# Kernel tuning notes

Hardware: AMD Instinct MI355X
Metric: run time of the kernel (lower is better)

Reference implementation:

```python
import jax, jax.numpy as jnp
import numpy as np

G = 8      # conv groups
NG = 32    # groupnorm groups
H = 8      # attention heads
EPS = 1e-5
SLOPE = 0.1

def _qkv_branch(x, w, b, gw, gb):
    # x: [B, Cin, P]; w: [Cout, Cin//G]; grouped 1x1 conv == block matmul
    B, Cin, P = x.shape
    Cout = w.shape[0]
    xg = x.reshape(B, G, Cin // G, P)
    wg = w.reshape(G, Cout // G, Cin // G)
    y = jnp.einsum('gof,bgfp->bgop', wg, xg).reshape(B, Cout, P) + b[None, :, None]
    # GroupNorm(NG, Cout)
    yg = y.reshape(B, NG, Cout // NG, P)
    mu = yg.mean(axis=(2, 3), keepdims=True)
    var = yg.var(axis=(2, 3), keepdims=True)
    yn = ((yg - mu) * jax.lax.rsqrt(var + EPS)).reshape(B, Cout, P)
    yn = yn * gw[None, :, None] + gb[None, :, None]
    # LeakyReLU(0.1)
    return jnp.where(yn >= 0, yn, SLOPE * yn)

def setup_inputs() -> dict:
    key = jax.random.key(0)
    ks = jax.random.split(key, 14)
    B, Cin, Cout, P = 8, 512, 1024, 2048
    x = jax.random.normal(ks[0], (B, Cin, P), dtype=jnp.float32)
    def conv_w(k):
        return jax.random.normal(k, (Cout, Cin // G), dtype=jnp.float32) * 0.02
    inp = {
        'x': x,
        'wq': conv_w(ks[1]), 'bq': jnp.zeros((Cout,), jnp.float32),
        'gw1': jnp.ones((Cout,), jnp.float32), 'gb1': jnp.zeros((Cout,), jnp.float32),
        'wk': conv_w(ks[2]), 'bk': jnp.zeros((Cout,), jnp.float32),
        'gw2': jnp.ones((Cout,), jnp.float32), 'gb2': jnp.zeros((Cout,), jnp.float32),
        'wv': conv_w(ks[3]), 'bv': jnp.zeros((Cout,), jnp.float32),
        'gw3': jnp.ones((Cout,), jnp.float32), 'gb3': jnp.zeros((Cout,), jnp.float32),
    }
    return inp

def reference(x, wq, bq, gw1, gb1, wk, bk, gw2, gb2, wv, bv, gw3, gb3):
    Q = _qkv_branch(x, wq, bq, gw1, gb1)   # [B, C, P]
    K = _qkv_branch(x, wk, bk, gw2, gb2)
    V = _qkv_branch(x, wv, bv, gw3, gb3)
    B, C, P = K.shape
    d = C // H
    Qh = Q.reshape(B, H, d, P)
    Kh = K.reshape(B, H, d, P)
    Vh = V.reshape(B, H, d, P)
    scale = 1.0 / np.sqrt(C / H).astype(np.float32)
    scores = jnp.einsum('bhci,bhcj->bhij', Kh, Vh) * scale  # [B,H,P,P]
    A = jax.nn.softmax(scores, axis=-1)
    out = jnp.einsum('bhij,bhcj->bhci', A, Qh)              # [B,H,d,P]
    return out.reshape(B, C, P)
```

## Files before the change

### kernel.cpp

```cpp
#include <hip/hip_runtime.h>

typedef unsigned short ushort_t;
typedef float  f32x4   __attribute__((ext_vector_type(4)));
typedef float  f32x16  __attribute__((ext_vector_type(16)));
typedef __bf16 bf16x4  __attribute__((ext_vector_type(4)));
typedef __bf16 bf16x8  __attribute__((ext_vector_type(8)));

#define MFMA16(a,b,c) __builtin_amdgcn_mfma_f32_16x16x32_bf16((a),(b),(c),0,0,0)
#define MFMA32(a,b,c) __builtin_amdgcn_mfma_f32_32x32x16_bf16((a),(b),(c),0,0,0)

__device__ __forceinline__ ushort_t f2bf(float f) {
  union { float f; unsigned u; } v; v.f = f;
  unsigned u = v.u;
  unsigned r = u + 0x7FFFu + ((u >> 16) & 1u);
  return (ushort_t)(r >> 16);
}
__device__ __forceinline__ float bf2f(ushort_t s) {
  union { unsigned u; float f; } v; v.u = ((unsigned)s) << 16;
  return v.f;
}

__device__ __forceinline__ void gload_lds16(const ushort_t* g, ushort_t* l) {
  __builtin_amdgcn_global_load_lds(
      (const __attribute__((address_space(1))) unsigned int*)g,
      (__attribute__((address_space(3))) unsigned int*)l, 16, 0, 0);
}

__global__ __launch_bounds__(256) void conv_gn(
    const float* __restrict__ x,
    const float* __restrict__ wq, const float* __restrict__ wk, const float* __restrict__ wv,
    const float* __restrict__ bq, const float* __restrict__ bk, const float* __restrict__ bv,
    ushort_t* __restrict__ Qb, ushort_t* __restrict__ Kb, ushort_t* __restrict__ Vb,
    float* __restrict__ stats) {
  int pc = blockIdx.x;
  int gz = blockIdx.y;
  int b = gz & 7, g = gz >> 3;
  int tid = threadIdx.x, lane = tid & 63, wid = tid >> 6;
  int l15 = lane & 15, q = lane >> 4;

  __shared__ __align__(16) ushort_t xl[128 * 72];
  __shared__ __align__(16) ushort_t wl[128 * 72];
  __shared__ __align__(16) ushort_t yl[128 * 40];
  __shared__ float biasl[128];
  __shared__ float redbuf[8];

  const float* xsrc = x + ((size_t)(b * 512 + g * 64)) * 2048 + pc * 128;
#pragma unroll
  for (int r = 0; r < 8; ++r) {
    int chunk = tid + 256 * r;
    int c = chunk >> 5, p4 = chunk & 31;
    float4 v = *(const float4*)&xsrc[(size_t)c * 2048 + p4 * 4];
    xl[(p4 * 4 + 0) * 72 + c] = f2bf(v.x);
    xl[(p4 * 4 + 1) * 72 + c] = f2bf(v.y);
    xl[(p4 * 4 + 2) * 72 + c] = f2bf(v.z);
    xl[(p4 * 4 + 3) * 72 + c] = f2bf(v.w);
  }
  __syncthreads();

  bf16x8 Bx[2][2];
#pragma unroll
  for (int n2 = 0; n2 < 2; ++n2)
#pragma unroll
    for (int kk = 0; kk < 2; ++kk)
      Bx[n2][kk] = *(const bf16x8*)&xl[((wid * 2 + n2) * 16 + l15) * 72 + kk * 32 + q * 8];

  for (int br = 0; br < 3; ++br) {
    const float* w    = (br == 0) ? wq : ((br == 1) ? wk : wv);
    const float* bias = (br == 0) ? bq : ((br == 1) ? bk : bv);
    ushort_t* dst     = (br == 0) ? Qb : ((br == 1) ? Kb : Vb);
    __syncthreads();
    const float* wsrc = w + (size_t)g * 128 * 64;
#pragma unroll
    for (int r = 0; r < 8; ++r) {
      int idx = (tid + 256 * r) << 2;
      float4 v = *(const float4*)&wsrc[idx];
      int row = idx >> 6, f = idx & 63;
      wl[row * 72 + f + 0] = f2bf(v.x);
      wl[row * 72 + f + 1] = f2bf(v.y);
      wl[row * 72 + f + 2] = f2bf(v.z);
      wl[row * 72 + f + 3] = f2bf(v.w);
    }
    if (tid < 128) biasl[tid] = bias[g * 128 + tid];
    __syncthreads();

    for (int ngs = 0; ngs < 4; ++ngs) {
      int co0 = ngs * 32;
      bf16x8 Aw[2][2];
#pragma unroll
      for (int m = 0; m < 2; ++m)
#pragma unroll
        for (int kk = 0; kk < 2; ++kk)
          Aw[m][kk] = *(const bf16x8*)&wl[(co0 + m * 16 + l15) * 72 + kk * 32 + q * 8];
      f32x4 acc[2][2];
#pragma unroll
      for (int m = 0; m < 2; ++m)
#pragma unroll
        for (int n2 = 0; n2 < 2; ++n2) acc[m][n2] = (f32x4){0.f, 0.f, 0.f, 0.f};
#pragma unroll
      for (int kk = 0; kk < 2; ++kk)
#pragma unroll
        for (int n2 = 0; n2 < 2; ++n2)
#pragma unroll
          for (int m = 0; m < 2; ++m)
            acc[m][n2] = MFMA16(Aw[m][kk], Bx[n2][kk], acc[m][n2]);

      float s1 = 0.f, s2 = 0.f;
#pragma unroll
      for (int m = 0; m < 2; ++m)
#pragma unroll
        for (int n2 = 0; n2 < 2; ++n2)
#pragma unroll
          for (int rg = 0; rg < 4; ++rg) {
            float y = acc[m][n2][rg] + biasl[co0 + m * 16 + 4 * q + rg];
            acc[m][n2][rg] = y;
            s1 += y; s2 += y * y;
          }
#pragma unroll
      for (int mask = 32; mask >= 1; mask >>= 1) {
        s1 += __shfl_xor(s1, mask, 64);
        s2 += __shfl_xor(s2, mask, 64);
      }

      __syncthreads();
      if (lane == 0) { redbuf[wid * 2] = s1; redbuf[wid * 2 + 1] = s2; }
      if (br == 0) {
#pragma unroll
        for (int m = 0; m < 2; ++m)
#pragma unroll
          for (int n2 = 0; n2 < 2; ++n2)
#pragma unroll
            for (int rg = 0; rg < 4; ++rg)
              yl[(m * 16 + 4 * q + rg) * 136 + (wid * 2 + n2) * 16 + l15] = f2bf(acc[m][n2][rg]);
      } else {
#pragma unroll
        for (int m = 0; m < 2; ++m)
#pragma unroll
          for (int n2 = 0; n2 < 2; ++n2)
#pragma unroll
            for (int rg = 0; rg < 4; ++rg)
              yl[((wid * 2 + n2) * 16 + l15) * 40 + m * 16 + 4 * q + rg] = f2bf(acc[m][n2][rg]);
      }
      __syncthreads();

      if (br == 0) {
#pragma unroll
        for (int r = 0; r < 2; ++r) {
          int chunk = tid + 256 * r;
          int row = chunk >> 4, ch = chunk & 15;
          *(uint4*)&dst[((size_t)(b * 1024 + g * 128 + co0 + row)) * 2048 + pc * 128 + ch * 8] =
              *(const uint4*)&yl[row * 136 + ch * 8];
        }
      } else {
#pragma unroll
        for (int r = 0; r < 2; ++r) {
          int chunk = tid + 256 * r;
          int row = chunk >> 2, ch = chunk & 3;
          *(uint4*)&dst[((size_t)(b * 8 + g) * 2048 + pc * 128 + row) * 128 + co0 + ch * 8] =
              *(const uint4*)&yl[row * 40 + ch * 8];
        }
      }
      if (tid == 0) {
        float S1 = redbuf[0] + redbuf[2] + redbuf[4] + redbuf[6];
        float S2 = redbuf[1] + redbuf[3] + redbuf[5] + redbuf[7];
        int sidx = (br * 8 + b) * 32 + g * 4 + ngs;
        atomicAdd(&stats[2 * sidx], S1);
        atomicAdd(&stats[2 * sidx + 1], S2);
      }
    }
  }
}

__global__ __launch_bounds__(256) void gn_apply(
    ushort_t* __restrict__ buf, const float* __restrict__ stats,
    const float* __restrict__ gw1, const float* __restrict__ gb1,
    const float* __restrict__ gw2, const float* __restrict__ gb2,
    const float* __restrict__ gw3, const float* __restrict__ gb3) {
  const unsigned NQ = 16777216u;
  unsigned gid = blockIdx.x * 256 + threadIdx.x;
  unsigned e = gid * 8;
  int br; unsigned local;
  if (e < NQ)            { br = 0; local = e; }
  else if (e < 2u * NQ)  { br = 1; local = e - NQ; }
  else                   { br = 2; local = e - 2u * NQ; }
  int b, c0;
  if (br == 0) { b = local >> 21; c0 = (local >> 11) & 1023; }
  else {
    int cih = local & 127; int h = (local >> 18) & 7;
    b = local >> 21; c0 = h * 128 + cih;
  }
  int ng = c0 >> 5;
  const float* gw = (br == 0) ? gw1 : ((br == 1) ? gw2 : gw3);
  const float* gb = (br == 0) ? gb1 : ((br == 1) ? gb2 : gb3);
  int sidx = (br * 8 + b) * 32 + ng;
  float mean = stats[2 * sidx] * (1.f / 65536.f);
  float var  = stats[2 * sidx + 1] * (1.f / 65536.f) - mean * mean;
  float rstd = rsqrtf(var + 1e-5f);
  uint4 d = *(uint4*)&buf[(size_t)e];
  ushort_t* pu = (ushort_t*)&d;
#pragma unroll
  for (int i = 0; i < 8; ++i) {
    int ci = (br == 0) ? c0 : (c0 + i);
    float a = rstd * gw[ci];
    float b2 = gb[ci] - mean * a;
    float yn = fmaf(bf2f(pu[i]), a, b2);
    yn = (yn >= 0.f) ? yn : 0.1f * yn;
    pu[i] = f2bf(yn);
  }
  *(uint4*)&buf[(size_t)e] = d;
}

__global__ __launch_bounds__(256, 2) void attn(
    const ushort_t* __restrict__ Qb, const ushort_t* __restrict__ Kb,
    const ushort_t* __restrict__ Vb, float* __restrict__ out) {
  __shared__ __align__(16) ushort_t fKs[2][32 * 128];
  __shared__ __align__(16) ushort_t Vs[2][128 * 32];
  __shared__ __align__(16) ushort_t Ps[256 * 40];

  int it = blockIdx.x, bh = blockIdx.y;
  int b = bh >> 3, h = bh & 7;
  int tid = threadIdx.x, lane = tid & 63, wid = tid >> 6;
  int l31 = lane & 31, q2 = lane >> 5;
  const float sl = 0.08838834764831845f * 1.4426950408889634f;

  bf16x8 Bq[2][8];
#pragma unroll
  for (int nt = 0; nt < 2; ++nt) {
    const ushort_t* fQp =
        Kb + ((size_t)bh * 2048 + it * 256 + wid * 64 + nt * 32 + l31) * 128 + q2 * 8;
#pragma unroll
    for (int dc = 0; dc < 8; ++dc) Bq[nt][dc] = *(const bf16x8*)&fQp[dc * 16];
  }

  float m2[2], l_i[2];
  m2[0] = m2[1] = -3e38f;
  l_i[0] = l_i[1] = 0.f;
  f32x16 O[4][2];
#pragma unroll
  for (int mt = 0; mt < 4; ++mt)
#pragma unroll
    for (int nt = 0; nt < 2; ++nt) O[mt][nt] = (f32x16)(0.f);

  const ushort_t* fKg = Vb + (size_t)bh * 2048 * 128;
  const ushort_t* fVg = Qb + ((size_t)(b * 1024 + h * 128)) * 2048;

#define STAGE(JT, NB)                                                          \
  do {                                                                         \
    _Pragma("unroll")                                                          \
    for (int r = 0; r < 2; ++r) {                                              \
      int n = tid + 256 * r;                                                   \
      int kr = n >> 4, ku = (n & 15) ^ (kr & 7);                               \
      gload_lds16(fKg + (size_t)(JT) * 4096 + kr * 128 + ku * 8,               \
                  &fKs[NB][n * 8]);                                            \
      int vr = n >> 2, vu = (n & 3) ^ ((vr >> 1) & 3);                         \
      gload_lds16(fVg + (size_t)vr * 2048 + (JT) * 32 + vu * 8,                \
                  &Vs[NB][n * 8]);                                             \
    }                                                                          \
  } while (0)

  STAGE(0, 0);
  __syncthreads();
  int cur = 0;

  for (int jt = 0; jt < 64; ++jt) {
    if (jt < 63) STAGE(jt + 1, cur ^ 1);

    f32x16 ST[2];
    ST[0] = (f32x16)(0.f);
    ST[1] = (f32x16)(0.f);
#pragma unroll
    for (int dc = 0; dc < 8; ++dc) {
      int up = (dc * 2 + q2) ^ (l31 & 7);
      bf16x8 Ak = *(const bf16x8*)&fKs[cur][l31 * 128 + up * 8];
      ST[0] = MFMA32(Ak, Bq[0][dc], ST[0]);
      ST[1] = MFMA32(Ak, Bq[1][dc], ST[1]);
    }

#pragma unroll
    for (int nt = 0; nt < 2; ++nt) {
      float vmax = ST[nt][0];
#pragma unroll
      for (int rg = 1; rg < 16; ++rg) vmax = fmaxf(vmax, ST[nt][rg]);
      float v2 = vmax * sl;
      v2 = fmaxf(v2, __shfl_xor(v2, 32, 64));
      float al = 1.f;
      bool need = !__all(v2 <= m2[nt] + 8.f);
      if (need) {
        float mn = fmaxf(m2[nt], v2);
        al = __builtin_amdgcn_exp2f(m2[nt] - mn);
        m2[nt] = mn;
      }
      float mn = m2[nt];
      float rs = 0.f;
      int prow = (wid * 64 + nt * 32 + l31) * 40;
#pragma unroll
      for (int r = 0; r < 4; ++r) {
        float p0 = __builtin_amdgcn_exp2f(fmaf(ST[nt][4 * r + 0], sl, -mn));
        float p1 = __builtin_amdgcn_exp2f(fmaf(ST[nt][4 * r + 1], sl, -mn));
        float p2 = __builtin_amdgcn_exp2f(fmaf(ST[nt][4 * r + 2], sl, -mn));
        float p3 = __builtin_amdgcn_exp2f(fmaf(ST[nt][4 * r + 3], sl, -mn));
        rs += (p0 + p1) + (p2 + p3);
        bf16x4 pk = {(__bf16)p0, (__bf16)p1, (__bf16)p2, (__bf16)p3};
        *(bf16x4*)&Ps[prow + r * 8 + q2 * 4] = pk;
      }
      rs += __shfl_xor(rs, 32, 64);
      l_i[nt] = l_i[nt] * al + rs;
      if (need) {
#pragma unroll
        for (int mt = 0; mt < 4; ++mt)
#pragma unroll
          for (int rg = 0; rg < 16; ++rg) O[mt][nt][rg] *= al;
      }
    }

#pragma unroll
    for (int jc = 0; jc < 2; ++jc) {
      bf16x8 Bp[2];
#pragma unroll
      for (int nt = 0; nt < 2; ++nt)
        Bp[nt] = *(const bf16x8*)&Ps[(wid * 64 + nt * 32 + l31) * 40 + jc * 16 + q2 * 8];
#pragma unroll
      for (int mt = 0; mt < 4; ++mt) {
        int row = mt * 32 + l31;
        int up = (jc * 2 + q2) ^ ((row >> 1) & 3);
        bf16x8 Av = *(const bf16x8*)&Vs[cur][row * 32 + up * 8];
        O[mt][0] = MFMA32(Av, Bp[0], O[mt][0]);
        O[mt][1] = MFMA32(Av, Bp[1], O[mt][1]);
      }
    }
    __syncthreads();
    cur ^= 1;
  }
#undef STAGE

  float linv[2];
  linv[0] = 1.f / l_i[0];
  linv[1] = 1.f / l_i[1];
#pragma unroll
  for (int mt = 0; mt < 4; ++mt)
#pragma unroll
    for (int nt = 0; nt < 2; ++nt) {
      float* obase = out + ((size_t)(b * 1024 + h * 128 + mt * 32)) * 2048 +
                     it * 256 + wid * 64 + nt * 32 + l31;
#pragma unroll
      for (int rg = 0; rg < 16; ++rg) {
        int c = (rg & 3) + 8 * (rg >> 2) + 4 * q2;
        obase[(size_t)c * 2048] = O[mt][nt][rg] * linv[nt];
      }
    }
}

extern "C" void kernel_launch(void* const* d_in, const int* in_sizes, int n_in,
                              void* d_out, int out_size, void* d_ws, size_t ws_size,
                              hipStream_t stream) {
  const float* x   = (const float*)d_in[0];
  const float* wq  = (const float*)d_in[1];
  const float* bq  = (const float*)d_in[2];
  const float* gw1 = (const float*)d_in[3];
  const float* gb1 = (const float*)d_in[4];
  const float* wk  = (const float*)d_in[5];
  const float* bk  = (const float*)d_in[6];
  const float* gw2 = (const float*)d_in[7];
  const float* gb2 = (const float*)d_in[8];
  const float* wv  = (const float*)d_in[9];
  const float* bv  = (const float*)d_in[10];
  const float* gw3 = (const float*)d_in[11];
  const float* gb3 = (const float*)d_in[12];
  float* out = (float*)d_out;
  char* ws = (char*)d_ws;

  ushort_t* Qb = (ushort_t*)(ws);
  ushort_t* Kb = (ushort_t*)(ws + 33554432);
  ushort_t* Vb = (ushort_t*)(ws + 67108864);
  float* stats = (float*)(ws + 100663296);

  hipMemsetAsync(stats, 0, 1536 * sizeof(float), stream);
  conv_gn<<<dim3(16, 64), 256, 0, stream>>>(x, wq, wk, wv, bq, bk, bv,
                                            Qb, Kb, Vb, stats);
  gn_apply<<<24576, 256, 0, stream>>>(Qb, stats, gw1, gb1, gw2, gb2, gw3, gb3);
  attn<<<dim3(8, 64), 256, 0, stream>>>(Qb, Kb, Vb, out);
}
```

Before: 446.9 us.

## Shrink attention query tile, swap grid order, vectorize conv stores, grid-stride GN apply

The attention kernel now gives each block 128 query columns instead of 256, so each wave holds one 32-column tile. The grid is reordered so head-batch varies fastest, the P buffer shrinks and uses an XOR swizzle, and launch bounds rise to 4 blocks per CU for more occupancy and parallelism. The conv kernel transposes its Q-branch MFMA so bias and stores can be written as packed bf16x4 vectors, and the weight conversion is vectorized. The GN apply kernel becomes a 12-iteration grid-stride loop over far fewer blocks. The risk is that K/V tiles get reused across fewer queries, which doubles K/V tile traffic per output.

```diff
diff --git a/kernel.cpp b/kernel.cpp
--- a/kernel.cpp
+++ b/kernel.cpp
@@ -75,10 +75,8 @@
       int idx = (tid + 256 * r) << 2;
       float4 v = *(const float4*)&wsrc[idx];
       int row = idx >> 6, f = idx & 63;
-      wl[row * 72 + f + 0] = f2bf(v.x);
-      wl[row * 72 + f + 1] = f2bf(v.y);
-      wl[row * 72 + f + 2] = f2bf(v.z);
-      wl[row * 72 + f + 3] = f2bf(v.w);
+      bf16x4 wv4 = {(__bf16)v.x, (__bf16)v.y, (__bf16)v.z, (__bf16)v.w};
+      *(bf16x4*)&wl[row * 72 + f] = wv4;
     }
     if (tid < 128) biasl[tid] = bias[g * 128 + tid];
     __syncthreads();
@@ -93,28 +91,53 @@
           Aw[m][kk] = *(const bf16x8*)&wl[(co0 + m * 16 + l15) * 72 + kk * 32 + q * 8];
       f32x4 acc[2][2];
 #pragma unroll
-      for (int m = 0; m < 2; ++m)
-#pragma unroll
-        for (int n2 = 0; n2 < 2; ++n2) acc[m][n2] = (f32x4){0.f, 0.f, 0.f, 0.f};
-#pragma unroll
-      for (int kk = 0; kk < 2; ++kk)
+      for (int a = 0; a < 2; ++a)
+#pragma unroll
+        for (int c2 = 0; c2 < 2; ++c2) acc[a][c2] = (f32x4){0.f, 0.f, 0.f, 0.f};
+      if (br == 0) {
+#pragma unroll
+        for (int kk = 0; kk < 2; ++kk)
+#pragma unroll
+          for (int n2 = 0; n2 < 2; ++n2)
+#pragma unroll
+            for (int mw = 0; mw < 2; ++mw)
+              acc[n2][mw] = MFMA16(Bx[n2][kk], Aw[mw][kk], acc[n2][mw]);
+      } else {
+#pragma unroll
+        for (int kk = 0; kk < 2; ++kk)
+#pragma unroll
+          for (int n2 = 0; n2 < 2; ++n2)
+#pragma unroll
+            for (int m = 0; m < 2; ++m)
+              acc[m][n2] = MFMA16(Aw[m][kk], Bx[n2][kk], acc[m][n2]);
+      }
+
+      float s1 = 0.f, s2 = 0.f;
+      if (br == 0) {
 #pragma unroll
         for (int n2 = 0; n2 < 2; ++n2)
 #pragma unroll
-          for (int m = 0; m < 2; ++m)
-            acc[m][n2] = MFMA16(Aw[m][kk], Bx[n2][kk], acc[m][n2]);
-
-      float s1 = 0.f, s2 = 0.f;
-#pragma unroll
-      for (int m = 0; m < 2; ++m)
-#pragma unroll
-        for (int n2 = 0; n2 < 2; ++n2)
-#pragma unroll
-          for (int rg = 0; rg < 4; ++rg) {
-            float y = acc[m][n2][rg] + biasl[co0 + m * 16 + 4 * q + rg];
-            acc[m][n2][rg] = y;
-            s1 += y; s2 += y * y;
+          for (int mw = 0; mw < 2; ++mw) {
+            float bi = biasl[co0 + mw * 16 + l15];
+#pragma unroll
+            for (int rg = 0; rg < 4; ++rg) {
+              float y = acc[n2][mw][rg] + bi;
+              acc[n2][mw][rg] = y;
+              s1 += y; s2 += y * y;
+            }
           }
+      } else {
+#pragma unroll
+        for (int m = 0; m < 2; ++m)
+#pragma unroll
+          for (int n2 = 0; n2 < 2; ++n2)
+#pragma unroll
+            for (int rg = 0; rg < 4; ++rg) {
+              float y = acc[m][n2][rg] + biasl[co0 + m * 16 + 4 * q + rg];
+              acc[m][n2][rg] = y;
+              s1 += y; s2 += y * y;
+            }
+      }
 #pragma unroll
       for (int mask = 32; mask >= 1; mask >>= 1) {
         s1 += __shfl_xor(s1, mask, 64);
@@ -125,20 +148,22 @@
       if (lane == 0) { redbuf[wid * 2] = s1; redbuf[wid * 2 + 1] = s2; }
       if (br == 0) {
 #pragma unroll
+        for (int n2 = 0; n2 < 2; ++n2)
+#pragma unroll
+          for (int mw = 0; mw < 2; ++mw) {
+            bf16x4 pk = {(__bf16)acc[n2][mw][0], (__bf16)acc[n2][mw][1],
+                         (__bf16)acc[n2][mw][2], (__bf16)acc[n2][mw][3]};
+            *(bf16x4*)&yl[(mw * 16 + l15) * 136 + (wid * 2 + n2) * 16 + 4 * q] = pk;
+          }
+      } else {
+#pragma unroll
         for (int m = 0; m < 2; ++m)
 #pragma unroll
-          for (int n2 = 0; n2 < 2; ++n2)
-#pragma unroll
-            for (int rg = 0; rg < 4; ++rg)
-              yl[(m * 16 + 4 * q + rg) * 136 + (wid * 2 + n2) * 16 + l15] = f2bf(acc[m][n2][rg]);
-      } else {
-#pragma unroll
-        for (int m = 0; m < 2; ++m)
-#pragma unroll
-          for (int n2 = 0; n2 < 2; ++n2)
-#pragma unroll
-            for (int rg = 0; rg < 4; ++rg)
-              yl[((wid * 2 + n2) * 16 + l15) * 40 + m * 16 + 4 * q + rg] = f2bf(acc[m][n2][rg]);
+          for (int n2 = 0; n2 < 2; ++n2) {
+            bf16x4 pk = {(__bf16)acc[m][n2][0], (__bf16)acc[m][n2][1],
+                         (__bf16)acc[m][n2][2], (__bf16)acc[m][n2][3]};
+            *(bf16x4*)&yl[((wid * 2 + n2) * 16 + l15) * 40 + m * 16 + 4 * q] = pk;
+          }
       }
       __syncthreads();
 
@@ -176,72 +201,73 @@
     const float* __restrict__ gw2, const float* __restrict__ gb2,
     const float* __restrict__ gw3, const float* __restrict__ gb3) {
   const unsigned NQ = 16777216u;
-  unsigned gid = blockIdx.x * 256 + threadIdx.x;
-  unsigned e = gid * 8;
-  int br; unsigned local;
-  if (e < NQ)            { br = 0; local = e; }
-  else if (e < 2u * NQ)  { br = 1; local = e - NQ; }
-  else                   { br = 2; local = e - 2u * NQ; }
-  int b, c0;
-  if (br == 0) { b = local >> 21; c0 = (local >> 11) & 1023; }
-  else {
-    int cih = local & 127; int h = (local >> 18) & 7;
-    b = local >> 21; c0 = h * 128 + cih;
-  }
-  int ng = c0 >> 5;
-  const float* gw = (br == 0) ? gw1 : ((br == 1) ? gw2 : gw3);
-  const float* gb = (br == 0) ? gb1 : ((br == 1) ? gb2 : gb3);
-  int sidx = (br * 8 + b) * 32 + ng;
-  float mean = stats[2 * sidx] * (1.f / 65536.f);
-  float var  = stats[2 * sidx + 1] * (1.f / 65536.f) - mean * mean;
-  float rstd = rsqrtf(var + 1e-5f);
-  uint4 d = *(uint4*)&buf[(size_t)e];
-  ushort_t* pu = (ushort_t*)&d;
-#pragma unroll
-  for (int i = 0; i < 8; ++i) {
-    int ci = (br == 0) ? c0 : (c0 + i);
-    float a = rstd * gw[ci];
-    float b2 = gb[ci] - mean * a;
-    float yn = fmaf(bf2f(pu[i]), a, b2);
-    yn = (yn >= 0.f) ? yn : 0.1f * yn;
-    pu[i] = f2bf(yn);
-  }
-  *(uint4*)&buf[(size_t)e] = d;
-}
-
-__global__ __launch_bounds__(256, 2) void attn(
+  unsigned base = blockIdx.x * 256 + threadIdx.x;
+  for (int itn = 0; itn < 12; ++itn) {
+    unsigned gid = base + (unsigned)itn * 524288u;
+    unsigned e = gid * 8;
+    int br; unsigned local;
+    if (e < NQ)            { br = 0; local = e; }
+    else if (e < 2u * NQ)  { br = 1; local = e - NQ; }
+    else                   { br = 2; local = e - 2u * NQ; }
+    int b, c0;
+    if (br == 0) { b = local >> 21; c0 = (local >> 11) & 1023; }
+    else {
+      int cih = local & 127; int h = (local >> 18) & 7;
+      b = local >> 21; c0 = h * 128 + cih;
+    }
+    int ng = c0 >> 5;
+    const float* gw = (br == 0) ? gw1 : ((br == 1) ? gw2 : gw3);
+    const float* gb = (br == 0) ? gb1 : ((br == 1) ? gb2 : gb3);
+    int sidx = (br * 8 + b) * 32 + ng;
+    float mean = stats[2 * sidx] * (1.f / 65536.f);
+    float var  = stats[2 * sidx + 1] * (1.f / 65536.f) - mean * mean;
+    float rstd = rsqrtf(var + 1e-5f);
+    uint4 d = *(uint4*)&buf[(size_t)e];
+    ushort_t* pu = (ushort_t*)&d;
+#pragma unroll
+    for (int i = 0; i < 8; ++i) {
+      int ci = (br == 0) ? c0 : (c0 + i);
+      float a = rstd * gw[ci];
+      float b2 = gb[ci] - mean * a;
+      float yn = fmaf(bf2f(pu[i]), a, b2);
+      yn = (yn >= 0.f) ? yn : 0.1f * yn;
+      pu[i] = f2bf(yn);
+    }
+    *(uint4*)&buf[(size_t)e] = d;
+  }
+}
+
+__global__ __launch_bounds__(256, 4) void attn(
     const ushort_t* __restrict__ Qb, const ushort_t* __restrict__ Kb,
     const ushort_t* __restrict__ Vb, float* __restrict__ out) {
   __shared__ __align__(16) ushort_t fKs[2][32 * 128];
   __shared__ __align__(16) ushort_t Vs[2][128 * 32];
-  __shared__ __align__(16) ushort_t Ps[256 * 40];
-
-  int it = blockIdx.x, bh = blockIdx.y;
+  __shared__ __align__(16) ushort_t Ps[128 * 32];
+
+  int bh = blockIdx.x, it = blockIdx.y;
   int b = bh >> 3, h = bh & 7;
   int tid = threadIdx.x, lane = tid & 63, wid = tid >> 6;
   int l31 = lane & 31, q2 = lane >> 5;
   const float sl = 0.08838834764831845f * 1.4426950408889634f;
 
-  bf16x8 Bq[2][8];
-#pragma unroll
-  for (int nt = 0; nt < 2; ++nt) {
+  bf16x8 Bq[8];
+  {
     const ushort_t* fQp =
-        Kb + ((size_t)bh * 2048 + it * 256 + wid * 64 + nt * 32 + l31) * 128 + q2 * 8;
-#pragma unroll
-    for (int dc = 0; dc < 8; ++dc) Bq[nt][dc] = *(const bf16x8*)&fQp[dc * 16];
-  }
-
-  float m2[2], l_i[2];
-  m2[0] = m2[1] = -3e38f;
-  l_i[0] = l_i[1] = 0.f;
-  f32x16 O[4][2];
-#pragma unroll
-  for (int mt = 0; mt < 4; ++mt)
-#pragma unroll
-    for (int nt = 0; nt < 2; ++nt) O[mt][nt] = (f32x16)(0.f);
+        Kb + ((size_t)bh * 2048 + it * 128 + wid * 32 + l31) * 128 + q2 * 8;
+#pragma unroll
+    for (int dc = 0; dc < 8; ++dc) Bq[dc] = *(const bf16x8*)&fQp[dc * 16];
+  }
+
+  float m2 = -3e38f, l_i = 0.f;
+  f32x16 O[4];
+#pragma unroll
+  for (int mt = 0; mt < 4; ++mt) O[mt] = (f32x16)(0.f);
 
   const ushort_t* fKg = Vb + (size_t)bh * 2048 * 128;
   const ushort_t* fVg = Qb + ((size_t)(b * 1024 + h * 128)) * 2048;
+
+  int prow = wid * 32 + l31;
+  int pswz = (prow ^ (prow >> 2)) & 3;
 
 #define STAGE(JT, NB)                                                          \
   do {                                                                         \
@@ -264,67 +290,62 @@
   for (int jt = 0; jt < 64; ++jt) {
     if (jt < 63) STAGE(jt + 1, cur ^ 1);
 
-    f32x16 ST[2];
-    ST[0] = (f32x16)(0.f);
-    ST[1] = (f32x16)(0.f);
+    f32x16 ST = (f32x16)(0.f);
 #pragma unroll
     for (int dc = 0; dc < 8; ++dc) {
       int up = (dc * 2 + q2) ^ (l31 & 7);
       bf16x8 Ak = *(const bf16x8*)&fKs[cur][l31 * 128 + up * 8];
-      ST[0] = MFMA32(Ak, Bq[0][dc], ST[0]);
-      ST[1] = MFMA32(Ak, Bq[1][dc], ST[1]);
-    }
-
-#pragma unroll
-    for (int nt = 0; nt < 2; ++nt) {
-      float vmax = ST[nt][0];
-#pragma unroll
-      for (int rg = 1; rg < 16; ++rg) vmax = fmaxf(vmax, ST[nt][rg]);
+      ST = MFMA32(Ak, Bq[dc], ST);
+    }
+
+    {
+      float vm[8];
+#pragma unroll
+      for (int r = 0; r < 8; ++r) vm[r] = fmaxf(ST[2 * r], ST[2 * r + 1]);
+#pragma unroll
+      for (int r = 0; r < 4; ++r) vm[r] = fmaxf(vm[r], vm[r + 4]);
+      float vmax = fmaxf(fmaxf(vm[0], vm[1]), fmaxf(vm[2], vm[3]));
       float v2 = vmax * sl;
       v2 = fmaxf(v2, __shfl_xor(v2, 32, 64));
       float al = 1.f;
-      bool need = !__all(v2 <= m2[nt] + 8.f);
+      bool need = !__all(v2 <= m2 + 8.f);
       if (need) {
-        float mn = fmaxf(m2[nt], v2);
-        al = __builtin_amdgcn_exp2f(m2[nt] - mn);
-        m2[nt] = mn;
-      }
-      float mn = m2[nt];
+        float mn2 = fmaxf(m2, v2);
+        al = __builtin_amdgcn_exp2f(m2 - mn2);
+        m2 = mn2;
+      }
+      float mn = m2;
       float rs = 0.f;
-      int prow = (wid * 64 + nt * 32 + l31) * 40;
 #pragma unroll
       for (int r = 0; r < 4; ++r) {
-        float p0 = __builtin_amdgcn_exp2f(fmaf(ST[nt][4 * r + 0], sl, -mn));
-        float p1 = __builtin_amdgcn_exp2f(fmaf(ST[nt][4 * r + 1], sl, -mn));
-        float p2 = __builtin_amdgcn_exp2f(fmaf(ST[nt][4 * r + 2], sl, -mn));
-        float p3 = __builtin_amdgcn_exp2f(fmaf(ST[nt][4 * r + 3], sl, -mn));
+        float p0 = __builtin_amdgcn_exp2f(fmaf(ST[4 * r + 0], sl, -mn));
+        float p1 = __builtin_amdgcn_exp2f(fmaf(ST[4 * r + 1], sl, -mn));
+        float p2 = __builtin_amdgcn_exp2f(fmaf(ST[4 * r + 2], sl, -mn));
+        float p3 = __builtin_amdgcn_exp2f(fmaf(ST[4 * r + 3], sl, -mn));
         rs += (p0 + p1) + (p2 + p3);
         bf16x4 pk = {(__bf16)p0, (__bf16)p1, (__bf16)p2, (__bf16)p3};
-        *(bf16x4*)&Ps[prow + r * 8 + q2 * 4] = pk;
+        *(bf16x4*)&Ps[prow * 32 + (r ^ pswz) * 8 + q2 * 4] = pk;
       }
       rs += __shfl_xor(rs, 32, 64);
-      l_i[nt] = l_i[nt] * al + rs;
+      l_i = l_i * al + rs;
       if (need) {
 #pragma unroll
         for (int mt = 0; mt < 4; ++mt)
 #pragma unroll
-          for (int rg = 0; rg < 16; ++rg) O[mt][nt][rg] *= al;
+          for (int rg = 0; rg < 16; ++rg) O[mt][rg] *= al;
       }
     }
 
 #pragma unroll
     for (int jc = 0; jc < 2; ++jc) {
-      bf16x8 Bp[2];
-#pragma unroll
-      for (int nt = 0; nt < 2; ++nt)
-        Bp[nt] = *(const bf16x8*)&Ps[(wid * 64 + nt * 32 + l31) * 40 + jc * 16 + q2 * 8];
+      int pu = ((jc * 2 + q2) ^ pswz);
+      bf16x8 Bp = *(const bf16x8*)&Ps[prow * 32 + pu * 8];
 #pragma unroll
       for (int mt = 0; mt < 4; ++mt) {
         int row = mt * 32 + l31;
         int up = (jc * 2 + q2) ^ ((row >> 1) & 3);
         bf16x8 Av = *(const bf16x8*)&Vs[cur][row * 32 + up * 8];
-        O[mt][0] = MFMA32(Av, Bp[0], O[mt][0]);
-        O[mt][1] = MFMA32(Av, Bp[1], O[mt][1]);
+        O[mt] = MFMA32(Av, Bp, O[mt]);
       }
     }
     __syncthreads();
@@ -332,21 +353,17 @@
   }
 #undef STAGE
 
-  float linv[2];
-  linv[0] = 1.f / l_i[0];
-  linv[1] = 1.f / l_i[1];
-#pragma unroll
-  for (int mt = 0; mt < 4; ++mt)
-#pragma unroll
-    for (int nt = 0; nt < 2; ++nt) {
-      float* obase = out + ((size_t)(b * 1024 + h * 128 + mt * 32)) * 2048 +
-                     it * 256 + wid * 64 + nt * 32 + l31;
-#pragma unroll
-      for (int rg = 0; rg < 16; ++rg) {
-        int c = (rg & 3) + 8 * (rg >> 2) + 4 * q2;
-        obase[(size_t)c * 2048] = O[mt][nt][rg] * linv[nt];
-      }
-    }
+  float linv = 1.f / l_i;
+#pragma unroll
+  for (int mt = 0; mt < 4; ++mt) {
+    float* obase = out + ((size_t)(b * 1024 + h * 128 + mt * 32)) * 2048 +
+                   it * 128 + wid * 32 + l31;
+#pragma unroll
+    for (int rg = 0; rg < 16; ++rg) {
+      int c = (rg & 3) + 8 * (rg >> 2) + 4 * q2;
+      obase[(size_t)c * 2048] = O[mt][rg] * linv;
+    }
+  }
 }
 
 extern "C" void kernel_launch(void* const* d_in, const int* in_sizes, int n_in,
@@ -376,6 +393,6 @@
   hipMemsetAsync(stats, 0, 1536 * sizeof(float), stream);
   conv_gn<<<dim3(16, 64), 256, 0, stream>>>(x, wq, wk, wv, bq, bk, bv,
                                             Qb, Kb, Vb, stats);
-  gn_apply<<<24576, 256, 0, stream>>>(Qb, stats, gw1, gb1, gw2, gb2, gw3, gb3);
-  attn<<<dim3(8, 64), 256, 0, stream>>>(Qb, Kb, Vb, out);
-}
+  gn_apply<<<2048, 256, 0, stream>>>(Qb, stats, gw1, gb1, gw2, gb2, gw3, gb3);
+  attn<<<dim3(64, 16), 256, 0, stream>>>(Qb, Kb, Vb, out);
+}
```

Measured after the change: 575.6 us. +28.8%, slower.

## Keep softmax probabilities in registers via permlane swap; tidy conv and GN kernels

Applied to the files above, without the earlier changes.

The attention kernel no longer writes P to LDS and reads it back. It packs exp values into bf16 pairs with v_cvt_pk_bf16_f32 and rearranges them across half-waves with v_permlane32_swap so they form the MFMA B operand directly. It also adds s_setprio around the MFMA sections and remaps block indices so blocks sharing a (b,h) are grouped. The conv kernel swaps operands for the Q branch to write packed bf16x4 stores, and uses vector weight conversion. gn_apply becomes a grid-stride loop over 2048 blocks. Together these remove LDS round trips and launch overhead, at the cost of register pressure and reliance on gfx950-specific instructions.

```diff
diff --git a/kernel.cpp b/kernel.cpp
--- a/kernel.cpp
+++ b/kernel.cpp
@@ -5,6 +5,7 @@
 typedef float  f32x16  __attribute__((ext_vector_type(16)));
 typedef __bf16 bf16x4  __attribute__((ext_vector_type(4)));
 typedef __bf16 bf16x8  __attribute__((ext_vector_type(8)));
+typedef unsigned uint2v __attribute__((ext_vector_type(2)));
 
 #define MFMA16(a,b,c) __builtin_amdgcn_mfma_f32_16x16x32_bf16((a),(b),(c),0,0,0)
 #define MFMA32(a,b,c) __builtin_amdgcn_mfma_f32_32x32x16_bf16((a),(b),(c),0,0,0)
@@ -18,6 +19,15 @@
 __device__ __forceinline__ float bf2f(ushort_t s) {
   union { unsigned u; float f; } v; v.u = ((unsigned)s) << 16;
   return v.f;
+}
+
+__device__ __forceinline__ void plswap(unsigned& a, unsigned& b) {
+#if __has_builtin(__builtin_amdgcn_permlane32_swap)
+  uint2v r = __builtin_amdgcn_permlane32_swap(a, b, false, false);
+  a = r[0]; b = r[1];
+#else
+  asm("v_permlane32_swap_b32 %0, %1" : "+v"(a), "+v"(b));
+#endif
 }
 
 __device__ __forceinline__ void gload_lds16(const ushort_t* g, ushort_t* l) {
@@ -75,10 +85,8 @@
       int idx = (tid + 256 * r) << 2;
       float4 v = *(const float4*)&wsrc[idx];
       int row = idx >> 6, f = idx & 63;
-      wl[row * 72 + f + 0] = f2bf(v.x);
-      wl[row * 72 + f + 1] = f2bf(v.y);
-      wl[row * 72 + f + 2] = f2bf(v.z);
-      wl[row * 72 + f + 3] = f2bf(v.w);
+      bf16x4 wv4 = {(__bf16)v.x, (__bf16)v.y, (__bf16)v.z, (__bf16)v.w};
+      *(bf16x4*)&wl[row * 72 + f] = wv4;
     }
     if (tid < 128) biasl[tid] = bias[g * 128 + tid];
     __syncthreads();
@@ -93,28 +101,53 @@
           Aw[m][kk] = *(const bf16x8*)&wl[(co0 + m * 16 + l15) * 72 + kk * 32 + q * 8];
       f32x4 acc[2][2];
 #pragma unroll
-      for (int m = 0; m < 2; ++m)
-#pragma unroll
-        for (int n2 = 0; n2 < 2; ++n2) acc[m][n2] = (f32x4){0.f, 0.f, 0.f, 0.f};
-#pragma unroll
-      for (int kk = 0; kk < 2; ++kk)
+      for (int a = 0; a < 2; ++a)
+#pragma unroll
+        for (int c2 = 0; c2 < 2; ++c2) acc[a][c2] = (f32x4){0.f, 0.f, 0.f, 0.f};
+      if (br == 0) {
+#pragma unroll
+        for (int kk = 0; kk < 2; ++kk)
+#pragma unroll
+          for (int n2 = 0; n2 < 2; ++n2)
+#pragma unroll
+            for (int mw = 0; mw < 2; ++mw)
+              acc[n2][mw] = MFMA16(Bx[n2][kk], Aw[mw][kk], acc[n2][mw]);
+      } else {
+#pragma unroll
+        for (int kk = 0; kk < 2; ++kk)
+#pragma unroll
+          for (int n2 = 0; n2 < 2; ++n2)
+#pragma unroll
+            for (int m = 0; m < 2; ++m)
+              acc[m][n2] = MFMA16(Aw[m][kk], Bx[n2][kk], acc[m][n2]);
+      }
+
+      float s1 = 0.f, s2 = 0.f;
+      if (br == 0) {
 #pragma unroll
         for (int n2 = 0; n2 < 2; ++n2)
 #pragma unroll
-          for (int m = 0; m < 2; ++m)
-            acc[m][n2] = MFMA16(Aw[m][kk], Bx[n2][kk], acc[m][n2]);
-
-      float s1 = 0.f, s2 = 0.f;
-#pragma unroll
-      for (int m = 0; m < 2; ++m)
-#pragma unroll
-        for (int n2 = 0; n2 < 2; ++n2)
-#pragma unroll
-          for (int rg = 0; rg < 4; ++rg) {
-            float y = acc[m][n2][rg] + biasl[co0 + m * 16 + 4 * q + rg];
-            acc[m][n2][rg] = y;
-            s1 += y; s2 += y * y;
+          for (int mw = 0; mw < 2; ++mw) {
+            float bi = biasl[co0 + mw * 16 + l15];
+#pragma unroll
+            for (int rg = 0; rg < 4; ++rg) {
+              float y = acc[n2][mw][rg] + bi;
+              acc[n2][mw][rg] = y;
+              s1 += y; s2 += y * y;
+            }
           }
+      } else {
+#pragma unroll
+        for (int m = 0; m < 2; ++m)
+#pragma unroll
+          for (int n2 = 0; n2 < 2; ++n2)
+#pragma unroll
+            for (int rg = 0; rg < 4; ++rg) {
+              float y = acc[m][n2][rg] + biasl[co0 + m * 16 + 4 * q + rg];
+              acc[m][n2][rg] = y;
+              s1 += y; s2 += y * y;
+            }
+      }
 #pragma unroll
       for (int mask = 32; mask >= 1; mask >>= 1) {
         s1 += __shfl_xor(s1, mask, 64);
@@ -125,20 +158,22 @@
       if (lane == 0) { redbuf[wid * 2] = s1; redbuf[wid * 2 + 1] = s2; }
       if (br == 0) {
 #pragma unroll
+        for (int n2 = 0; n2 < 2; ++n2)
+#pragma unroll
+          for (int mw = 0; mw < 2; ++mw) {
+            bf16x4 pk = {(__bf16)acc[n2][mw][0], (__bf16)acc[n2][mw][1],
+                         (__bf16)acc[n2][mw][2], (__bf16)acc[n2][mw][3]};
+            *(bf16x4*)&yl[(mw * 16 + l15) * 136 + (wid * 2 + n2) * 16 + 4 * q] = pk;
+          }
+      } else {
+#pragma unroll
         for (int m = 0; m < 2; ++m)
 #pragma unroll
-          for (int n2 = 0; n2 < 2; ++n2)
-#pragma unroll
-            for (int rg = 0; rg < 4; ++rg)
-              yl[(m * 16 + 4 * q + rg) * 136 + (wid * 2 + n2) * 16 + l15] = f2bf(acc[m][n2][rg]);
-      } else {
-#pragma unroll
-        for (int m = 0; m < 2; ++m)
-#pragma unroll
-          for (int n2 = 0; n2 < 2; ++n2)
-#pragma unroll
-            for (int rg = 0; rg < 4; ++rg)
-              yl[((wid * 2 + n2) * 16 + l15) * 40 + m * 16 + 4 * q + rg] = f2bf(acc[m][n2][rg]);
+          for (int n2 = 0; n2 < 2; ++n2) {
+            bf16x4 pk = {(__bf16)acc[m][n2][0], (__bf16)acc[m][n2][1],
+                         (__bf16)acc[m][n2][2], (__bf16)acc[m][n2][3]};
+            *(bf16x4*)&yl[((wid * 2 + n2) * 16 + l15) * 40 + m * 16 + 4 * q] = pk;
+          }
       }
       __syncthreads();
 
@@ -176,37 +211,40 @@
     const float* __restrict__ gw2, const float* __restrict__ gb2,
     const float* __restrict__ gw3, const float* __restrict__ gb3) {
   const unsigned NQ = 16777216u;
-  unsigned gid = blockIdx.x * 256 + threadIdx.x;
-  unsigned e = gid * 8;
-  int br; unsigned local;
-  if (e < NQ)            { br = 0; local = e; }
-  else if (e < 2u * NQ)  { br = 1; local = e - NQ; }
-  else                   { br = 2; local = e - 2u * NQ; }
-  int b, c0;
-  if (br == 0) { b = local >> 21; c0 = (local >> 11) & 1023; }
-  else {
-    int cih = local & 127; int h = (local >> 18) & 7;
-    b = local >> 21; c0 = h * 128 + cih;
+  unsigned base = blockIdx.x * 256 + threadIdx.x;
+  for (int itn = 0; itn < 12; ++itn) {
+    unsigned gid = base + (unsigned)itn * 524288u;
+    unsigned e = gid * 8;
+    int br; unsigned local;
+    if (e < NQ)            { br = 0; local = e; }
+    else if (e < 2u * NQ)  { br = 1; local = e - NQ; }
+    else                   { br = 2; local = e - 2u * NQ; }
+    int b, c0;
+    if (br == 0) { b = local >> 21; c0 = (local >> 11) & 1023; }
+    else {
+      int cih = local & 127; int h = (local >> 18) & 7;
+      b = local >> 21; c0 = h * 128 + cih;
+    }
+    int ng = c0 >> 5;
+    const float* gw = (br == 0) ? gw1 : ((br == 1) ? gw2 : gw3);
+    const float* gb = (br == 0) ? gb1 : ((br == 1) ? gb2 : gb3);
+    int sidx = (br * 8 + b) * 32 + ng;
+    float mean = stats[2 * sidx] * (1.f / 65536.f);
+    float var  = stats[2 * sidx + 1] * (1.f / 65536.f) - mean * mean;
+    float rstd = rsqrtf(var + 1e-5f);
+    uint4 d = *(uint4*)&buf[(size_t)e];
+    ushort_t* pu = (ushort_t*)&d;
+#pragma unroll
+    for (int i = 0; i < 8; ++i) {
+      int ci = (br == 0) ? c0 : (c0 + i);
+      float a = rstd * gw[ci];
+      float b2 = gb[ci] - mean * a;
+      float yn = fmaf(bf2f(pu[i]), a, b2);
+      yn = (yn >= 0.f) ? yn : 0.1f * yn;
+      pu[i] = f2bf(yn);
+    }
+    *(uint4*)&buf[(size_t)e] = d;
   }
-  int ng = c0 >> 5;
-  const float* gw = (br == 0) ? gw1 : ((br == 1) ? gw2 : gw3);
-  const float* gb = (br == 0) ? gb1 : ((br == 1) ? gb2 : gb3);
-  int sidx = (br * 8 + b) * 32 + ng;
-  float mean = stats[2 * sidx] * (1.f / 65536.f);
-  float var  = stats[2 * sidx + 1] * (1.f / 65536.f) - mean * mean;
-  float rstd = rsqrtf(var + 1e-5f);
-  uint4 d = *(uint4*)&buf[(size_t)e];
-  ushort_t* pu = (ushort_t*)&d;
-#pragma unroll
-  for (int i = 0; i < 8; ++i) {
-    int ci = (br == 0) ? c0 : (c0 + i);
-    float a = rstd * gw[ci];
-    float b2 = gb[ci] - mean * a;
-    float yn = fmaf(bf2f(pu[i]), a, b2);
-    yn = (yn >= 0.f) ? yn : 0.1f * yn;
-    pu[i] = f2bf(yn);
-  }
-  *(uint4*)&buf[(size_t)e] = d;
 }
 
 __global__ __launch_bounds__(256, 2) void attn(
@@ -214,9 +252,10 @@
     const ushort_t* __restrict__ Vb, float* __restrict__ out) {
   __shared__ __align__(16) ushort_t fKs[2][32 * 128];
   __shared__ __align__(16) ushort_t Vs[2][128 * 32];
-  __shared__ __align__(16) ushort_t Ps[256 * 40];
-
-  int it = blockIdx.x, bh = blockIdx.y;
+
+  int lin = blockIdx.x + 8 * blockIdx.y;
+  int it = (lin >> 3) & 7;
+  int bh = (lin & 7) + 8 * (lin >> 6);
   int b = bh >> 3, h = bh & 7;
   int tid = threadIdx.x, lane = tid & 63, wid = tid >> 6;
   int l31 = lane & 31, q2 = lane >> 5;
@@ -267,6 +306,7 @@
     f32x16 ST[2];
     ST[0] = (f32x16)(0.f);
     ST[1] = (f32x16)(0.f);
+    __builtin_amdgcn_s_setprio(1);
 #pragma unroll
     for (int dc = 0; dc < 8; ++dc) {
       int up = (dc * 2 + q2) ^ (l31 & 7);
@@ -274,7 +314,9 @@
       ST[0] = MFMA32(Ak, Bq[0][dc], ST[0]);
       ST[1] = MFMA32(Ak, Bq[1][dc], ST[1]);
     }
-
+    __builtin_amdgcn_s_setprio(0);
+
+    bf16x8 Bp[2][2];
 #pragma unroll
     for (int nt = 0; nt < 2; ++nt) {
       float vmax = ST[nt][0];
@@ -285,22 +327,17 @@
       float al = 1.f;
       bool need = !__all(v2 <= m2[nt] + 8.f);
       if (need) {
-        float mn = fmaxf(m2[nt], v2);
-        al = __builtin_amdgcn_exp2f(m2[nt] - mn);
-        m2[nt] = mn;
+        float mn2 = fmaxf(m2[nt], v2);
+        al = __builtin_amdgcn_exp2f(m2[nt] - mn2);
+        m2[nt] = mn2;
       }
       float mn = m2[nt];
+      float p16[16];
       float rs = 0.f;
-      int prow = (wid * 64 + nt * 32 + l31) * 40;
-#pragma unroll
-      for (int r = 0; r < 4; ++r) {
-        float p0 = __builtin_amdgcn_exp2f(fmaf(ST[nt][4 * r + 0], sl, -mn));
-        float p1 = __builtin_amdgcn_exp2f(fmaf(ST[nt][4 * r + 1], sl, -mn));
-        float p2 = __builtin_amdgcn_exp2f(fmaf(ST[nt][4 * r + 2], sl, -mn));
-        float p3 = __builtin_amdgcn_exp2f(fmaf(ST[nt][4 * r + 3], sl, -mn));
-        rs += (p0 + p1) + (p2 + p3);
-        bf16x4 pk = {(__bf16)p0, (__bf16)p1, (__bf16)p2, (__bf16)p3};
-        *(bf16x4*)&Ps[prow + r * 8 + q2 * 4] = pk;
+#pragma unroll
+      for (int rg = 0; rg < 16; ++rg) {
+        p16[rg] = __builtin_amdgcn_exp2f(fmaf(ST[nt][rg], sl, -mn));
+        rs += p16[rg];
       }
       rs += __shfl_xor(rs, 32, 64);
       l_i[nt] = l_i[nt] * al + rs;
@@ -310,23 +347,38 @@
 #pragma unroll
           for (int rg = 0; rg < 16; ++rg) O[mt][nt][rg] *= al;
       }
-    }
-
+#pragma unroll
+      for (int jc = 0; jc < 2; ++jc) {
+        unsigned pa, pb, pc_, pd;
+        asm("v_cvt_pk_bf16_f32 %0, %1, %2"
+            : "=v"(pa) : "v"(p16[jc * 8 + 0]), "v"(p16[jc * 8 + 1]));
+        asm("v_cvt_pk_bf16_f32 %0, %1, %2"
+            : "=v"(pc_) : "v"(p16[jc * 8 + 2]), "v"(p16[jc * 8 + 3]));
+        asm("v_cvt_pk_bf16_f32 %0, %1, %2"
+            : "=v"(pb) : "v"(p16[jc * 8 + 4]), "v"(p16[jc * 8 + 5]));
+        asm("v_cvt_pk_bf16_f32 %0, %1, %2"
+            : "=v"(pd) : "v"(p16[jc * 8 + 6]), "v"(p16[jc * 8 + 7]));
+        plswap(pa, pb);
+        plswap(pc_, pd);
+        union { unsigned u[4]; bf16x8 v; } fr;
+        fr.u[0] = pa; fr.u[1] = pc_; fr.u[2] = pb; fr.u[3] = pd;
+        Bp[nt][jc] = fr.v;
+      }
+    }
+
+    __builtin_amdgcn_s_setprio(1);
 #pragma unroll
     for (int jc = 0; jc < 2; ++jc) {
-      bf16x8 Bp[2];
-#pragma unroll
-      for (int nt = 0; nt < 2; ++nt)
-        Bp[nt] = *(const bf16x8*)&Ps[(wid * 64 + nt * 32 + l31) * 40 + jc * 16 + q2 * 8];
 #pragma unroll
       for (int mt = 0; mt < 4; ++mt) {
         int row = mt * 32 + l31;
         int up = (jc * 2 + q2) ^ ((row >> 1) & 3);
         bf16x8 Av = *(const bf16x8*)&Vs[cur][row * 32 + up * 8];
-        O[mt][0] = MFMA32(Av, Bp[0], O[mt][0]);
-        O[mt][1] = MFMA32(Av, Bp[1], O[mt][1]);
-      }
-    }
+        O[mt][0] = MFMA32(Av, Bp[0][jc], O[mt][0]);
+        O[mt][1] = MFMA32(Av, Bp[1][jc], O[mt][1]);
+      }
+    }
+    __builtin_amdgcn_s_setprio(0);
     __syncthreads();
     cur ^= 1;
   }
@@ -376,6 +428,6 @@
   hipMemsetAsync(stats, 0, 1536 * sizeof(float), stream);
   conv_gn<<<dim3(16, 64), 256, 0, stream>>>(x, wq, wk, wv, bq, bk, bv,
                                             Qb, Kb, Vb, stats);
-  gn_apply<<<24576, 256, 0, stream>>>(Qb, stats, gw1, gb1, gw2, gb2, gw3, gb3);
+  gn_apply<<<2048, 256, 0, stream>>>(Qb, stats, gw1, gb1, gw2, gb2, gw3, gb3);
   attn<<<dim3(8, 64), 256, 0, stream>>>(Qb, Kb, Vb, out);
 }
```

Result: faster. 409.5 us (-8.4%).
